# Performance work log

Measured on AMD Instinct MI355X. Metric: run time of the kernel, lower is better.

## Reference

```python
import jax, jax.numpy as jnp
import numpy as np

N_NODES = 100000
N_EDGES = 1600000
IN_DIM, HID_DIM, OUT_DIM = 128, 128, 64


def setup_inputs() -> dict:
    key = jax.random.key(0)
    ks = jax.random.split(key, 8)
    x = jax.random.normal(ks[0], (N_NODES, IN_DIM), dtype=jnp.float32)
    edge_index = jax.random.randint(ks[1], (2, N_EDGES), 0, N_NODES, dtype=jnp.int64)
    sc = 0.05
    W1 = jax.random.normal(ks[2], (IN_DIM, HID_DIM), dtype=jnp.float32) * sc
    b1 = jnp.zeros((HID_DIM,), dtype=jnp.float32)
    W2 = jax.random.normal(ks[3], (HID_DIM, HID_DIM), dtype=jnp.float32) * sc
    b2 = jnp.zeros((HID_DIM,), dtype=jnp.float32)
    W3 = jax.random.normal(ks[4], (HID_DIM, OUT_DIM), dtype=jnp.float32) * sc
    b3 = jnp.zeros((OUT_DIM,), dtype=jnp.float32)
    return {"x": x, "edge_index": edge_index, "W1": W1, "b1": b1,
            "W2": W2, "b2": b2, "W3": W3, "b3": b3}


def _gcn_conv(x, src, dst, norm, W, b, n_nodes):
    # x' = D^{-1/2} (A + I) D^{-1/2} (x W) + b   (PyG GCNConv default)
    h = x @ W                                   # [N, F_out]
    msg = h[src] * norm[:, None]                # gather + scale, [E+N, F_out]
    agg = jax.ops.segment_sum(msg, dst, num_segments=n_nodes)  # scatter-add
    return agg + b


def _build_norm(edge_index, n_nodes):
    # add self-loops, compute symmetric normalization coefficients
    loops = jnp.arange(n_nodes, dtype=edge_index.dtype)
    src = jnp.concatenate([edge_index[0], loops])
    dst = jnp.concatenate([edge_index[1], loops])
    deg = jax.ops.segment_sum(jnp.ones_like(dst, dtype=jnp.float32), dst,
                              num_segments=n_nodes)
    dinv = jnp.where(deg > 0, jax.lax.rsqrt(jnp.maximum(deg, 1.0)), 0.0)
    norm = dinv[src] * dinv[dst]
    return src, dst, norm


def reference(x, edge_index, W1, b1, W2, b2, W3, b3):
    n = x.shape[0]
    src, dst, norm = _build_norm(edge_index, n)
    h = jax.nn.relu(_gcn_conv(x, src, dst, norm, W1, b1, n))
    h = jax.nn.relu(_gcn_conv(h, src, dst, norm, W2, b2, n))
    out = _gcn_conv(h, src, dst, norm, W3, b3, n)
    return out
```

## Files before the change

### kernel.cpp

```cpp
#include <hip/hip_runtime.h>
#include <hip/hip_fp16.h>
#include <cstdint>
#include <cstddef>
#include <type_traits>

#define NN 100000
#define NE 1600000
#define SCAN_BLOCKS ((NN + 1023) / 1024)
#define NBK ((NN + 255) / 256)
#define BCAP 4608
#define EPB 4096
#define BIN_BLOCKS ((NE + EPB - 1) / EPB)

using half8 = __attribute__((ext_vector_type(8))) _Float16;
using f32x4 = __attribute__((ext_vector_type(4))) float;

union F4H8 { float4 f4; __half2 h2[4]; };

__device__ __forceinline__ uint2 pack4half(float4 v) {
    __half2 a = __floats2half2_rn(v.x, v.y);
    __half2 b = __floats2half2_rn(v.z, v.w);
    uint2 r;
    r.x = *(unsigned int*)&a;
    r.y = *(unsigned int*)&b;
    return r;
}

__global__ void detect_flag_kernel(const int* __restrict__ idx, int* __restrict__ flag) {
    __shared__ int cnt;
    if (threadIdx.x == 0) cnt = 0;
    __syncthreads();
    if (idx[2 * threadIdx.x + 1] == 0) atomicAdd(&cnt, 1);
    __syncthreads();
    if (threadIdx.x == 0) *flag = (cnt == (int)blockDim.x) ? 1 : 0;
}

__global__ __launch_bounds__(256) void bin_kernel(const void* __restrict__ idx,
                                                  const int* __restrict__ flag,
                                                  int* __restrict__ gcnt,
                                                  int* __restrict__ bucketbuf) {
    __shared__ int cnt[NBK];
    __shared__ int gbase[NBK];
    int t = threadIdx.x;
    long long base = (long long)blockIdx.x * EPB;
    for (int i = t; i < NBK; i += 256) cnt[i] = 0;
    __syncthreads();
    bool is64 = (*flag != 0);
    int lpos[16];
#pragma unroll
    for (int j = 0; j < 16; j++) {
        long long e = base + j * 256 + t;
        lpos[j] = 0;
        if (e < NE) {
            int d_ = is64 ? (int)((const long long*)idx)[NE + e]
                          : ((const int*)idx)[NE + e];
            lpos[j] = atomicAdd(&cnt[d_ >> 8], 1);
        }
    }
    __syncthreads();
    for (int b = t; b < NBK; b += 256) {
        int c = cnt[b];
        gbase[b] = (c > 0) ? atomicAdd(&gcnt[b * 16], c) : 0;
    }
    __syncthreads();
#pragma unroll
    for (int j = 0; j < 16; j++) {
        long long e = base + j * 256 + t;
        if (e < NE) {
            int s_, d_;
            if (is64) { const long long* p = (const long long*)idx; s_ = (int)p[e]; d_ = (int)p[NE + e]; }
            else      { const int* p = (const int*)idx;             s_ = p[e];      d_ = p[NE + e]; }
            int b = d_ >> 8;
            int pos = gbase[b] + lpos[j];
            if (pos < BCAP) bucketbuf[(size_t)b * BCAP + pos] = (s_ << 8) | (d_ & 255);
        }
    }
}

__global__ __launch_bounds__(256) void hist_kernel(const int* __restrict__ gcnt,
                                                   const int* __restrict__ bucketbuf,
                                                   int* __restrict__ deg) {
    __shared__ int cnt[256];
    int t = threadIdx.x, b = blockIdx.x;
    cnt[t] = 0;
    __syncthreads();
    int n = gcnt[b * 16]; if (n > BCAP) n = BCAP;
    for (int i = t; i < n; i += 256)
        atomicAdd(&cnt[bucketbuf[(size_t)b * BCAP + i] & 255], 1);
    __syncthreads();
    int node = b * 256 + t;
    if (node < NN) deg[node] = cnt[t];
}

__global__ void dinv_kernel(const int* __restrict__ deg, float* __restrict__ dinv) {
    int n = blockIdx.x * blockDim.x + threadIdx.x;
    if (n < NN) dinv[n] = rsqrtf((float)(deg[n] + 1));
}

__global__ __launch_bounds__(256) void scanA_kernel(const int* __restrict__ deg,
                                                    int* __restrict__ blocksum) {
    __shared__ int red[256];
    int t = threadIdx.x;
    int base = blockIdx.x * 1024 + t * 4;
    int s = 0;
#pragma unroll
    for (int j = 0; j < 4; j++) { int i = base + j; if (i < NN) s += deg[i]; }
    red[t] = s;
    __syncthreads();
    for (int off = 128; off > 0; off >>= 1) {
        if (t < off) red[t] += red[t + off];
        __syncthreads();
    }
    if (t == 0) blocksum[blockIdx.x] = red[0];
}

__global__ __launch_bounds__(256) void scanC_kernel(const int* __restrict__ deg,
                                                    const int* __restrict__ blocksum,
                                                    int* __restrict__ row_start) {
    __shared__ int lds[256];
    __shared__ int boff_s;
    int t = threadIdx.x;
    int b = blockIdx.x;
    lds[t] = (t < b && t < SCAN_BLOCKS) ? blocksum[t] : 0;
    __syncthreads();
    for (int off = 128; off > 0; off >>= 1) {
        if (t < off) lds[t] += lds[t + off];
        __syncthreads();
    }
    if (t == 0) boff_s = lds[0];
    __syncthreads();
    int boff = boff_s;

    int base = b * 1024 + t * 4;
    int d[4]; int s = 0;
#pragma unroll
    for (int j = 0; j < 4; j++) { int i = base + j; d[j] = (i < NN) ? deg[i] : 0; s += d[j]; }
    __syncthreads();
    lds[t] = s;
    __syncthreads();
    for (int off = 1; off < 256; off <<= 1) {
        int u = (t >= off) ? lds[t - off] : 0;
        __syncthreads();
        lds[t] += u;
        __syncthreads();
    }
    int offr = boff + ((t == 0) ? 0 : lds[t - 1]);
#pragma unroll
    for (int j = 0; j < 4; j++) {
        int i = base + j;
        if (i < NN) { row_start[i] = offr; offr += d[j]; }
    }
    if (b == 0 && t == 0) row_start[NN] = NE;
}

__global__ __launch_bounds__(256) void csrfill_kernel(const int* __restrict__ gcnt,
                                                      const int* __restrict__ bucketbuf,
                                                      const int* __restrict__ row_start,
                                                      int* __restrict__ csr) {
    __shared__ int cur[256];
    int t = threadIdx.x, b = blockIdx.x;
    int node = b * 256 + t;
    cur[t] = (node < NN) ? row_start[node] : 0;
    __syncthreads();
    int n = gcnt[b * 16]; if (n > BCAP) n = BCAP;
    for (int i = t; i < n; i += 256) {
        int v = bucketbuf[(size_t)b * BCAP + i];
        int pos = atomicAdd(&cur[v & 255], 1);
        csr[pos] = v >> 8;
    }
}

__global__ void wt_kernel(const float* __restrict__ W, __half* __restrict__ Wt, int F) {
    int i = blockIdx.x * 256 + threadIdx.x;
    if (i >= 128 * F) return;
    int k = i / F, n = i % F;
    Wt[(size_t)n * 128 + k] = __float2half(W[i]);
}

__global__ void xh_kernel(const float* __restrict__ X, __half* __restrict__ Xh) {
    int i = blockIdx.x * 256 + threadIdx.x;
    if (i >= NN * 128 / 4) return;
    float4 v = ((const float4*)X)[i];
    *(uint2*)&Xh[(size_t)i * 4] = pack4half(v);
}

template <int F>
__global__ __launch_bounds__(256) void mfma_gemm_kernel(const __half* __restrict__ A,
                                                        const __half* __restrict__ Wt,
                                                        const float* __restrict__ dinv,
                                                        __half* __restrict__ H, int N) {
    constexpr int K = 128;
    constexpr int NT = F / 16;
    constexpr int FP = F + 8;
    __shared__ __half hs[64 * FP];

    int wave = threadIdx.x >> 6;
    int lane = threadIdx.x & 63;
    int quad = lane >> 4;
    int l16  = lane & 15;
    int rowbase = blockIdx.x * 64 + wave * 16;
    int arow = rowbase + l16; if (arow >= N) arow = N - 1;

    half8 afrag[4];
    const __half* ap = A + (size_t)arow * K + quad * 8;
#pragma unroll
    for (int s = 0; s < 4; s++) afrag[s] = *(const half8*)(ap + s * 32);

    f32x4 acc[NT];
#pragma unroll
    for (int t = 0; t < NT; t++) acc[t] = (f32x4){0.f, 0.f, 0.f, 0.f};

#pragma unroll
    for (int s = 0; s < 4; s++) {
#pragma unroll
        for (int t = 0; t < NT; t++) {
            half8 b = *(const half8*)(Wt + (size_t)(t * 16 + l16) * K + s * 32 + quad * 8);
            acc[t] = __builtin_amdgcn_mfma_f32_16x16x32_f16(afrag[s], b, acc[t], 0, 0, 0);
        }
    }

    float dv[4];
#pragma unroll
    for (int r = 0; r < 4; r++) {
        int grow = rowbase + quad * 4 + r;
        dv[r] = (grow < N) ? dinv[grow] : 0.f;
    }
#pragma unroll
    for (int t = 0; t < NT; t++) {
#pragma unroll
        for (int r = 0; r < 4; r++) {
            int lrow = wave * 16 + quad * 4 + r;
            hs[lrow * FP + t * 16 + l16] = __float2half(acc[t][r] * dv[r]);
        }
    }
    __syncthreads();
    constexpr int CHUNKS = 64 * F / 8;
    for (int i = threadIdx.x; i < CHUNKS; i += 256) {
        int row = i / (F / 8);
        int col8 = (i % (F / 8)) * 8;
        int grow = blockIdx.x * 64 + row;
        if (grow < N)
            *(uint4*)&H[(size_t)grow * F + col8] = *(const uint4*)&hs[row * FP + col8];
    }
}

template <int F, bool RELU, typename OutT>
__global__ __launch_bounds__(256) void agg_kernel(const __half* __restrict__ Hs,
                                                  const int* __restrict__ rs,
                                                  const int* __restrict__ csr,
                                                  const float* __restrict__ dinv,
                                                  const float* __restrict__ bias,
                                                  OutT* __restrict__ OUT) {
    constexpr int CQ = F / 8;
    constexpr int NPB = 256 / CQ;
    int node = blockIdx.x * NPB + threadIdx.x / CQ;
    int q = (threadIdx.x % CQ) * 8;
    if (node >= NN) return;
    float dn = dinv[node];
    float acc[8];
    {
        F4H8 u; u.f4 = *(const float4*)&Hs[(size_t)node * F + q];
#pragma unroll
        for (int j = 0; j < 4; j++) {
            float2 f = __half22float2(u.h2[j]);
            acc[2 * j] = f.x; acc[2 * j + 1] = f.y;
        }
    }
    int e = rs[node];
    int e1 = rs[node + 1];
    for (; e + 8 <= e1; e += 8) {
        int s[8];
#pragma unroll
        for (int j = 0; j < 8; j++) s[j] = csr[e + j];
        F4H8 h[8];
#pragma unroll
        for (int j = 0; j < 8; j++) h[j].f4 = *(const float4*)&Hs[(size_t)s[j] * F + q];
#pragma unroll
        for (int j = 0; j < 8; j++) {
#pragma unroll
            for (int k = 0; k < 4; k++) {
                float2 f = __half22float2(h[j].h2[k]);
                acc[2 * k] += f.x; acc[2 * k + 1] += f.y;
            }
        }
    }
    for (; e < e1; e++) {
        int s = csr[e];
        F4H8 u; u.f4 = *(const float4*)&Hs[(size_t)s * F + q];
#pragma unroll
        for (int k = 0; k < 4; k++) {
            float2 f = __half22float2(u.h2[k]);
            acc[2 * k] += f.x; acc[2 * k + 1] += f.y;
        }
    }
    float o[8];
#pragma unroll
    for (int j = 0; j < 8; j++) {
        o[j] = dn * acc[j] + bias[q + j];
        if (RELU) o[j] = fmaxf(o[j], 0.f);
    }
    if constexpr (std::is_same<OutT, float>::value) {
        *(float4*)&OUT[(size_t)node * F + q]     = make_float4(o[0], o[1], o[2], o[3]);
        *(float4*)&OUT[(size_t)node * F + q + 4] = make_float4(o[4], o[5], o[6], o[7]);
    } else {
        uint4 p;
        uint2 a = pack4half(make_float4(o[0], o[1], o[2], o[3]));
        uint2 b = pack4half(make_float4(o[4], o[5], o[6], o[7]));
        p.x = a.x; p.y = a.y; p.z = b.x; p.w = b.y;
        *(uint4*)&OUT[(size_t)node * F + q] = p;
    }
}

extern "C" void kernel_launch(void* const* d_in, const int* in_sizes, int n_in,
                              void* d_out, int out_size, void* d_ws, size_t ws_size,
                              hipStream_t stream) {
    const float* x  = (const float*)d_in[0];
    const void* eidx = d_in[1];
    const float* W1 = (const float*)d_in[2];
    const float* b1 = (const float*)d_in[3];
    const float* W2 = (const float*)d_in[4];
    const float* b2 = (const float*)d_in[5];
    const float* W3 = (const float*)d_in[6];
    const float* b3 = (const float*)d_in[7];
    float* out = (float*)d_out;

    char* ws = (char*)d_ws;
    size_t off = 0;
    auto alloc = [&](size_t bytes) -> void* {
        void* p = ws + off;
        off += (bytes + 255) & ~(size_t)255;
        return p;
    };
    __half* bufB = (__half*)alloc((size_t)NN * 128 * 2);
    int* deg      = (int*)bufB;
    int* blocksum = (int*)((char*)bufB + (size_t)NN * 4);
    int* row_start = (int*)alloc((size_t)(NN + 1) * 4);
    float* dinv = (float*)alloc((size_t)NN * 4);
    int* flagp  = (int*)alloc(256);
    int* csr    = (int*)alloc((size_t)NE * 4);
    __half* bufH = (__half*)alloc((size_t)NN * 128 * 2);
    int* bucketbuf = (int*)bufH;
    int* gcnt      = (int*)((char*)bufH + (size_t)NBK * BCAP * 4);
    __half* Xh  = (__half*)alloc((size_t)NN * 128 * 2);
    __half* Wt1 = (__half*)alloc((size_t)128 * 128 * 2);
    __half* Wt2 = (__half*)alloc((size_t)128 * 128 * 2);
    __half* Wt3 = (__half*)alloc((size_t)64 * 128 * 2);

    hipMemsetAsync(gcnt, 0, (size_t)NBK * 16 * 4, stream);
    detect_flag_kernel<<<1, 256, 0, stream>>>((const int*)eidx, flagp);
    bin_kernel<<<BIN_BLOCKS, 256, 0, stream>>>(eidx, flagp, gcnt, bucketbuf);
    hist_kernel<<<NBK, 256, 0, stream>>>(gcnt, bucketbuf, deg);
    dinv_kernel<<<(NN + 255) / 256, 256, 0, stream>>>(deg, dinv);
    scanA_kernel<<<SCAN_BLOCKS, 256, 0, stream>>>(deg, blocksum);
    scanC_kernel<<<SCAN_BLOCKS, 256, 0, stream>>>(deg, blocksum, row_start);
    csrfill_kernel<<<NBK, 256, 0, stream>>>(gcnt, bucketbuf, row_start, csr);

    wt_kernel<<<(128 * 128 + 255) / 256, 256, 0, stream>>>(W1, Wt1, 128);
    wt_kernel<<<(128 * 128 + 255) / 256, 256, 0, stream>>>(W2, Wt2, 128);
    wt_kernel<<<(128 * 64 + 255) / 256, 256, 0, stream>>>(W3, Wt3, 64);
    xh_kernel<<<(NN * 128 / 4 + 255) / 256, 256, 0, stream>>>(x, Xh);

    const int GB = (NN + 63) / 64;
    mfma_gemm_kernel<128><<<GB, 256, 0, stream>>>(Xh, Wt1, dinv, bufH, NN);
    agg_kernel<128, true, __half><<<NN / 16, 256, 0, stream>>>(bufH, row_start, csr, dinv, b1, bufB);
    mfma_gemm_kernel<128><<<GB, 256, 0, stream>>>(bufB, Wt2, dinv, bufH, NN);
    agg_kernel<128, true, __half><<<NN / 16, 256, 0, stream>>>(bufH, row_start, csr, dinv, b2, bufB);
    mfma_gemm_kernel<64><<<GB, 256, 0, stream>>>(bufB, Wt3, dinv, bufH, NN);
    agg_kernel<64, false, float><<<NN / 32, 256, 0, stream>>>(bufH, row_start, csr, dinv, b3, out);
}
```

Measured before the change: 426.9 us.

## Sort nodes by degree for aggregation, fuse fp32 input conversion into GEMM

Builds a degree-bucketed node permutation (counting sort over 64 degree bins) during preprocessing. All three aggregation kernels then process nodes in that order, which reduces divergence among threads of a wave that handle nodes with different edge counts. The separate x-to-fp16 conversion pass is removed and the first GEMM reads fp32 directly and converts in registers. The dinv computation is also folded into the histogram kernel, and bin_kernel keeps dst indices in registers instead of reloading them. The cost is two extra small kernels plus an indirect order lookup, and output writes that are no longer coalesced across neighbouring nodes.

After: 424.8 us. No clear change (-0.5%).

```diff
diff --git a/kernel.cpp b/kernel.cpp
--- a/kernel.cpp
+++ b/kernel.cpp
@@ -11,6 +11,7 @@
 #define BCAP 4608
 #define EPB 4096
 #define BIN_BLOCKS ((NE + EPB - 1) / EPB)
+#define SBINS 64
 
 using half8 = __attribute__((ext_vector_type(8))) _Float16;
 using f32x4 = __attribute__((ext_vector_type(4))) float;
@@ -46,14 +47,15 @@
     for (int i = t; i < NBK; i += 256) cnt[i] = 0;
     __syncthreads();
     bool is64 = (*flag != 0);
-    int lpos[16];
+    int lpos[16], d16[16];
 #pragma unroll
     for (int j = 0; j < 16; j++) {
         long long e = base + j * 256 + t;
-        lpos[j] = 0;
+        lpos[j] = 0; d16[j] = 0;
         if (e < NE) {
             int d_ = is64 ? (int)((const long long*)idx)[NE + e]
                           : ((const int*)idx)[NE + e];
+            d16[j] = d_;
             lpos[j] = atomicAdd(&cnt[d_ >> 8], 1);
         }
     }
@@ -67,9 +69,8 @@
     for (int j = 0; j < 16; j++) {
         long long e = base + j * 256 + t;
         if (e < NE) {
-            int s_, d_;
-            if (is64) { const long long* p = (const long long*)idx; s_ = (int)p[e]; d_ = (int)p[NE + e]; }
-            else      { const int* p = (const int*)idx;             s_ = p[e];      d_ = p[NE + e]; }
+            int s_ = is64 ? (int)((const long long*)idx)[e] : ((const int*)idx)[e];
+            int d_ = d16[j];
             int b = d_ >> 8;
             int pos = gbase[b] + lpos[j];
             if (pos < BCAP) bucketbuf[(size_t)b * BCAP + pos] = (s_ << 8) | (d_ & 255);
@@ -79,22 +80,28 @@
 
 __global__ __launch_bounds__(256) void hist_kernel(const int* __restrict__ gcnt,
                                                    const int* __restrict__ bucketbuf,
-                                                   int* __restrict__ deg) {
+                                                   int* __restrict__ deg,
+                                                   float* __restrict__ dinv,
+                                                   int* __restrict__ scnt) {
     __shared__ int cnt[256];
+    __shared__ int sh[SBINS];
     int t = threadIdx.x, b = blockIdx.x;
     cnt[t] = 0;
+    if (t < SBINS) sh[t] = 0;
     __syncthreads();
     int n = gcnt[b * 16]; if (n > BCAP) n = BCAP;
     for (int i = t; i < n; i += 256)
         atomicAdd(&cnt[bucketbuf[(size_t)b * BCAP + i] & 255], 1);
     __syncthreads();
     int node = b * 256 + t;
-    if (node < NN) deg[node] = cnt[t];
-}
-
-__global__ void dinv_kernel(const int* __restrict__ deg, float* __restrict__ dinv) {
-    int n = blockIdx.x * blockDim.x + threadIdx.x;
-    if (n < NN) dinv[n] = rsqrtf((float)(deg[n] + 1));
+    if (node < NN) {
+        int d = cnt[t];
+        deg[node] = d;
+        dinv[node] = rsqrtf((float)(d + 1));
+        atomicAdd(&sh[d < SBINS ? d : SBINS - 1], 1);
+    }
+    __syncthreads();
+    if (t < SBINS && sh[t] > 0) atomicAdd(&scnt[t * 16], sh[t]);
 }
 
 __global__ __launch_bounds__(256) void scanA_kernel(const int* __restrict__ deg,
@@ -170,6 +177,38 @@
     }
 }
 
+__global__ void sort_scan_kernel(const int* __restrict__ scnt, int* __restrict__ sbase) {
+    if (threadIdx.x == 0) {
+        int acc = 0;
+        for (int i = 0; i < SBINS; i++) { sbase[i * 16] = acc; acc += scnt[i * 16]; }
+    }
+}
+
+__global__ __launch_bounds__(256) void order_kernel(const int* __restrict__ deg,
+                                                    int* __restrict__ sbase,
+                                                    int* __restrict__ order) {
+    __shared__ int lcnt[SBINS];
+    __shared__ int lbase[SBINS];
+    int t = threadIdx.x;
+    if (t < SBINS) lcnt[t] = 0;
+    __syncthreads();
+    int node = blockIdx.x * 256 + t;
+    int bin = 0, lpos = 0;
+    bool valid = node < NN;
+    if (valid) {
+        int d = deg[node];
+        bin = d < SBINS ? d : SBINS - 1;
+        lpos = atomicAdd(&lcnt[bin], 1);
+    }
+    __syncthreads();
+    if (t < SBINS) {
+        int c = lcnt[t];
+        lbase[t] = (c > 0) ? atomicAdd(&sbase[t * 16], c) : 0;
+    }
+    __syncthreads();
+    if (valid) order[lbase[bin] + lpos] = node;
+}
+
 __global__ void wt_kernel(const float* __restrict__ W, __half* __restrict__ Wt, int F) {
     int i = blockIdx.x * 256 + threadIdx.x;
     if (i >= 128 * F) return;
@@ -177,15 +216,8 @@
     Wt[(size_t)n * 128 + k] = __float2half(W[i]);
 }
 
-__global__ void xh_kernel(const float* __restrict__ X, __half* __restrict__ Xh) {
-    int i = blockIdx.x * 256 + threadIdx.x;
-    if (i >= NN * 128 / 4) return;
-    float4 v = ((const float4*)X)[i];
-    *(uint2*)&Xh[(size_t)i * 4] = pack4half(v);
-}
-
-template <int F>
-__global__ __launch_bounds__(256) void mfma_gemm_kernel(const __half* __restrict__ A,
+template <int F, typename AT>
+__global__ __launch_bounds__(256) void mfma_gemm_kernel(const AT* __restrict__ A,
                                                         const __half* __restrict__ Wt,
                                                         const float* __restrict__ dinv,
                                                         __half* __restrict__ H, int N) {
@@ -202,9 +234,22 @@
     int arow = rowbase + l16; if (arow >= N) arow = N - 1;
 
     half8 afrag[4];
-    const __half* ap = A + (size_t)arow * K + quad * 8;
-#pragma unroll
-    for (int s = 0; s < 4; s++) afrag[s] = *(const half8*)(ap + s * 32);
+    const AT* ap = A + (size_t)arow * K + quad * 8;
+#pragma unroll
+    for (int s = 0; s < 4; s++) {
+        if constexpr (std::is_same<AT, float>::value) {
+            float4 u0 = *(const float4*)(ap + s * 32);
+            float4 u1 = *(const float4*)(ap + s * 32 + 4);
+            half8 h;
+            h[0] = (_Float16)u0.x; h[1] = (_Float16)u0.y;
+            h[2] = (_Float16)u0.z; h[3] = (_Float16)u0.w;
+            h[4] = (_Float16)u1.x; h[5] = (_Float16)u1.y;
+            h[6] = (_Float16)u1.z; h[7] = (_Float16)u1.w;
+            afrag[s] = h;
+        } else {
+            afrag[s] = *(const half8*)(ap + s * 32);
+        }
+    }
 
     f32x4 acc[NT];
 #pragma unroll
@@ -246,6 +291,7 @@
 
 template <int F, bool RELU, typename OutT>
 __global__ __launch_bounds__(256) void agg_kernel(const __half* __restrict__ Hs,
+                                                  const int* __restrict__ order,
                                                   const int* __restrict__ rs,
                                                   const int* __restrict__ csr,
                                                   const float* __restrict__ dinv,
@@ -253,9 +299,10 @@
                                                   OutT* __restrict__ OUT) {
     constexpr int CQ = F / 8;
     constexpr int NPB = 256 / CQ;
-    int node = blockIdx.x * NPB + threadIdx.x / CQ;
+    int idx = blockIdx.x * NPB + threadIdx.x / CQ;
     int q = (threadIdx.x % CQ) * 8;
-    if (node >= NN) return;
+    if (idx >= NN) return;
+    int node = order[idx];
     float dn = dinv[node];
     float acc[8];
     {
@@ -341,30 +388,33 @@
     __half* bufH = (__half*)alloc((size_t)NN * 128 * 2);
     int* bucketbuf = (int*)bufH;
     int* gcnt      = (int*)((char*)bufH + (size_t)NBK * BCAP * 4);
-    __half* Xh  = (__half*)alloc((size_t)NN * 128 * 2);
     __half* Wt1 = (__half*)alloc((size_t)128 * 128 * 2);
     __half* Wt2 = (__half*)alloc((size_t)128 * 128 * 2);
     __half* Wt3 = (__half*)alloc((size_t)64 * 128 * 2);
+    int* scnt  = (int*)alloc(SBINS * 16 * 4);
+    int* sbase = (int*)alloc(SBINS * 16 * 4);
+    int* order = (int*)alloc((size_t)NN * 4);
 
     hipMemsetAsync(gcnt, 0, (size_t)NBK * 16 * 4, stream);
+    hipMemsetAsync(scnt, 0, SBINS * 16 * 4, stream);
     detect_flag_kernel<<<1, 256, 0, stream>>>((const int*)eidx, flagp);
     bin_kernel<<<BIN_BLOCKS, 256, 0, stream>>>(eidx, flagp, gcnt, bucketbuf);
-    hist_kernel<<<NBK, 256, 0, stream>>>(gcnt, bucketbuf, deg);
-    dinv_kernel<<<(NN + 255) / 256, 256, 0, stream>>>(deg, dinv);
+    hist_kernel<<<NBK, 256, 0, stream>>>(gcnt, bucketbuf, deg, dinv, scnt);
     scanA_kernel<<<SCAN_BLOCKS, 256, 0, stream>>>(deg, blocksum);
     scanC_kernel<<<SCAN_BLOCKS, 256, 0, stream>>>(deg, blocksum, row_start);
     csrfill_kernel<<<NBK, 256, 0, stream>>>(gcnt, bucketbuf, row_start, csr);
+    sort_scan_kernel<<<1, 64, 0, stream>>>(scnt, sbase);
+    order_kernel<<<NBK, 256, 0, stream>>>(deg, sbase, order);
 
     wt_kernel<<<(128 * 128 + 255) / 256, 256, 0, stream>>>(W1, Wt1, 128);
     wt_kernel<<<(128 * 128 + 255) / 256, 256, 0, stream>>>(W2, Wt2, 128);
     wt_kernel<<<(128 * 64 + 255) / 256, 256, 0, stream>>>(W3, Wt3, 64);
-    xh_kernel<<<(NN * 128 / 4 + 255) / 256, 256, 0, stream>>>(x, Xh);
 
     const int GB = (NN + 63) / 64;
-    mfma_gemm_kernel<128><<<GB, 256, 0, stream>>>(Xh, Wt1, dinv, bufH, NN);
-    agg_kernel<128, true, __half><<<NN / 16, 256, 0, stream>>>(bufH, row_start, csr, dinv, b1, bufB);
-    mfma_gemm_kernel<128><<<GB, 256, 0, stream>>>(bufB, Wt2, dinv, bufH, NN);
-    agg_kernel<128, true, __half><<<NN / 16, 256, 0, stream>>>(bufH, row_start, csr, dinv, b2, bufB);
-    mfma_gemm_kernel<64><<<GB, 256, 0, stream>>>(bufB, Wt3, dinv, bufH, NN);
-    agg_kernel<64, false, float><<<NN / 32, 256, 0, stream>>>(bufH, row_start, csr, dinv, b3, out);
-}
+    mfma_gemm_kernel<128, float><<<GB, 256, 0, stream>>>(x, Wt1, dinv, bufH, NN);
+    agg_kernel<128, true, __half><<<NN / 16, 256, 0, stream>>>(bufH, order, row_start, csr, dinv, b1, bufB);
+    mfma_gemm_kernel<128, __half><<<GB, 256, 0, stream>>>(bufB, Wt2, dinv, bufH, NN);
+    agg_kernel<128, true, __half><<<NN / 16, 256, 0, stream>>>(bufH, order, row_start, csr, dinv, b2, bufB);
+    mfma_gemm_kernel<64, __half><<<GB, 256, 0, stream>>>(bufB, Wt3, dinv, bufH, NN);
+    agg_kernel<64, false, float><<<NN / 32, 256, 0, stream>>>(bufH, order, row_start, csr, dinv, b3, out);
+}
```

## Fuse aggregation with next-layer GEMM and fold fp16 conversion into first GEMM

Applied to the files above, without the earlier changes.

Hidden-layer aggregation is fused with the following layer's MFMA GEMM. Aggregated rows are staged in LDS, so the intermediate activation never makes a round trip through global memory. The x-to-fp16 conversion kernel is removed by converting fp32 rows inside the first GEMM's fragment load, and the dinv computation is folded into the histogram kernel. The bin kernel now keeps src/dst in registers instead of reloading them. The cost is a fused kernel that runs 64 nodes per block with 16 threads per node doing the gather, which may lower occupancy and memory-level parallelism compared with the standalone aggregation kernel.

New measurement: 398.8 us. 6.6% less time.

```diff
diff --git a/kernel.cpp b/kernel.cpp
--- a/kernel.cpp
+++ b/kernel.cpp
@@ -46,40 +46,40 @@
     for (int i = t; i < NBK; i += 256) cnt[i] = 0;
     __syncthreads();
     bool is64 = (*flag != 0);
-    int lpos[16];
+    int lpos[16], d16[16], s16[16];
 #pragma unroll
     for (int j = 0; j < 16; j++) {
         long long e = base + j * 256 + t;
-        lpos[j] = 0;
-        if (e < NE) {
-            int d_ = is64 ? (int)((const long long*)idx)[NE + e]
-                          : ((const int*)idx)[NE + e];
-            lpos[j] = atomicAdd(&cnt[d_ >> 8], 1);
-        }
-    }
-    __syncthreads();
-    for (int b = t; b < NBK; b += 256) {
-        int c = cnt[b];
-        gbase[b] = (c > 0) ? atomicAdd(&gcnt[b * 16], c) : 0;
-    }
-    __syncthreads();
-#pragma unroll
-    for (int j = 0; j < 16; j++) {
-        long long e = base + j * 256 + t;
+        lpos[j] = 0; d16[j] = 0; s16[j] = 0;
         if (e < NE) {
             int s_, d_;
             if (is64) { const long long* p = (const long long*)idx; s_ = (int)p[e]; d_ = (int)p[NE + e]; }
             else      { const int* p = (const int*)idx;             s_ = p[e];      d_ = p[NE + e]; }
-            int b = d_ >> 8;
+            d16[j] = d_; s16[j] = s_;
+            lpos[j] = atomicAdd(&cnt[d_ >> 8], 1);
+        }
+    }
+    __syncthreads();
+    for (int b = t; b < NBK; b += 256) {
+        int c = cnt[b];
+        gbase[b] = (c > 0) ? atomicAdd(&gcnt[b * 16], c) : 0;
+    }
+    __syncthreads();
+#pragma unroll
+    for (int j = 0; j < 16; j++) {
+        long long e = base + j * 256 + t;
+        if (e < NE) {
+            int b = d16[j] >> 8;
             int pos = gbase[b] + lpos[j];
-            if (pos < BCAP) bucketbuf[(size_t)b * BCAP + pos] = (s_ << 8) | (d_ & 255);
+            if (pos < BCAP) bucketbuf[(size_t)b * BCAP + pos] = (s16[j] << 8) | (d16[j] & 255);
         }
     }
 }
 
 __global__ __launch_bounds__(256) void hist_kernel(const int* __restrict__ gcnt,
                                                    const int* __restrict__ bucketbuf,
-                                                   int* __restrict__ deg) {
+                                                   int* __restrict__ deg,
+                                                   float* __restrict__ dinv) {
     __shared__ int cnt[256];
     int t = threadIdx.x, b = blockIdx.x;
     cnt[t] = 0;
@@ -89,12 +89,11 @@
         atomicAdd(&cnt[bucketbuf[(size_t)b * BCAP + i] & 255], 1);
     __syncthreads();
     int node = b * 256 + t;
-    if (node < NN) deg[node] = cnt[t];
-}
-
-__global__ void dinv_kernel(const int* __restrict__ deg, float* __restrict__ dinv) {
-    int n = blockIdx.x * blockDim.x + threadIdx.x;
-    if (n < NN) dinv[n] = rsqrtf((float)(deg[n] + 1));
+    if (node < NN) {
+        int d = cnt[t];
+        deg[node] = d;
+        dinv[node] = rsqrtf((float)(d + 1));
+    }
 }
 
 __global__ __launch_bounds__(256) void scanA_kernel(const int* __restrict__ deg,
@@ -177,15 +176,8 @@
     Wt[(size_t)n * 128 + k] = __float2half(W[i]);
 }
 
-__global__ void xh_kernel(const float* __restrict__ X, __half* __restrict__ Xh) {
-    int i = blockIdx.x * 256 + threadIdx.x;
-    if (i >= NN * 128 / 4) return;
-    float4 v = ((const float4*)X)[i];
-    *(uint2*)&Xh[(size_t)i * 4] = pack4half(v);
-}
-
-template <int F>
-__global__ __launch_bounds__(256) void mfma_gemm_kernel(const __half* __restrict__ A,
+template <int F, typename AT>
+__global__ __launch_bounds__(256) void mfma_gemm_kernel(const AT* __restrict__ A,
                                                         const __half* __restrict__ Wt,
                                                         const float* __restrict__ dinv,
                                                         __half* __restrict__ H, int N) {
@@ -202,9 +194,22 @@
     int arow = rowbase + l16; if (arow >= N) arow = N - 1;
 
     half8 afrag[4];
-    const __half* ap = A + (size_t)arow * K + quad * 8;
-#pragma unroll
-    for (int s = 0; s < 4; s++) afrag[s] = *(const half8*)(ap + s * 32);
+    const AT* ap = A + (size_t)arow * K + quad * 8;
+#pragma unroll
+    for (int s = 0; s < 4; s++) {
+        if constexpr (std::is_same<AT, float>::value) {
+            float4 u0 = *(const float4*)(ap + s * 32);
+            float4 u1 = *(const float4*)(ap + s * 32 + 4);
+            half8 h;
+            h[0] = (_Float16)u0.x; h[1] = (_Float16)u0.y;
+            h[2] = (_Float16)u0.z; h[3] = (_Float16)u0.w;
+            h[4] = (_Float16)u1.x; h[5] = (_Float16)u1.y;
+            h[6] = (_Float16)u1.z; h[7] = (_Float16)u1.w;
+            afrag[s] = h;
+        } else {
+            afrag[s] = *(const half8*)(ap + s * 32);
+        }
+    }
 
     f32x4 acc[NT];
 #pragma unroll
@@ -244,13 +249,135 @@
     }
 }
 
-template <int F, bool RELU, typename OutT>
+template <int FO>
+__global__ __launch_bounds__(256) void agg_gemm_kernel(const __half* __restrict__ Hs,
+                                                       const int* __restrict__ rs,
+                                                       const int* __restrict__ csr,
+                                                       const float* __restrict__ dinv,
+                                                       const float* __restrict__ bias,
+                                                       const __half* __restrict__ Wt,
+                                                       __half* __restrict__ Hout) {
+    constexpr int FI = 128;
+    constexpr int FP = FI + 8;
+    constexpr int NT = FO / 16;
+    __shared__ __half Alds[64 * FP];
+
+    int tid = threadIdx.x;
+    int nodebase = blockIdx.x * 64;
+
+#pragma unroll
+    for (int pass = 0; pass < 4; pass++) {
+        int lrow = pass * 16 + tid / 16;
+        int node = nodebase + lrow;
+        int q = (tid % 16) * 8;
+        float acc[8];
+        if (node < NN) {
+            float dn = dinv[node];
+            {
+                F4H8 u; u.f4 = *(const float4*)&Hs[(size_t)node * FI + q];
+#pragma unroll
+                for (int j = 0; j < 4; j++) {
+                    float2 f = __half22float2(u.h2[j]);
+                    acc[2 * j] = f.x; acc[2 * j + 1] = f.y;
+                }
+            }
+            int e = rs[node];
+            int e1 = rs[node + 1];
+            for (; e + 8 <= e1; e += 8) {
+                int s[8];
+#pragma unroll
+                for (int j = 0; j < 8; j++) s[j] = csr[e + j];
+                F4H8 h[8];
+#pragma unroll
+                for (int j = 0; j < 8; j++) h[j].f4 = *(const float4*)&Hs[(size_t)s[j] * FI + q];
+#pragma unroll
+                for (int j = 0; j < 8; j++) {
+#pragma unroll
+                    for (int k = 0; k < 4; k++) {
+                        float2 f = __half22float2(h[j].h2[k]);
+                        acc[2 * k] += f.x; acc[2 * k + 1] += f.y;
+                    }
+                }
+            }
+            for (; e < e1; e++) {
+                int s = csr[e];
+                F4H8 u; u.f4 = *(const float4*)&Hs[(size_t)s * FI + q];
+#pragma unroll
+                for (int k = 0; k < 4; k++) {
+                    float2 f = __half22float2(u.h2[k]);
+                    acc[2 * k] += f.x; acc[2 * k + 1] += f.y;
+                }
+            }
+#pragma unroll
+            for (int j = 0; j < 8; j++)
+                acc[j] = fmaxf(dn * acc[j] + bias[q + j], 0.f);
+        } else {
+#pragma unroll
+            for (int j = 0; j < 8; j++) acc[j] = 0.f;
+        }
+        uint4 p;
+        uint2 a = pack4half(make_float4(acc[0], acc[1], acc[2], acc[3]));
+        uint2 b = pack4half(make_float4(acc[4], acc[5], acc[6], acc[7]));
+        p.x = a.x; p.y = a.y; p.z = b.x; p.w = b.y;
+        *(uint4*)&Alds[lrow * FP + q] = p;
+    }
+    __syncthreads();
+
+    int wave = tid >> 6;
+    int lane = tid & 63;
+    int quad = lane >> 4;
+    int l16  = lane & 15;
+    int rowbase = nodebase + wave * 16;
+
+    half8 afrag[4];
+#pragma unroll
+    for (int s = 0; s < 4; s++)
+        afrag[s] = *(const half8*)&Alds[(wave * 16 + l16) * FP + s * 32 + quad * 8];
+
+    f32x4 acc[NT];
+#pragma unroll
+    for (int t = 0; t < NT; t++) acc[t] = (f32x4){0.f, 0.f, 0.f, 0.f};
+#pragma unroll
+    for (int s = 0; s < 4; s++) {
+#pragma unroll
+        for (int t = 0; t < NT; t++) {
+            half8 b = *(const half8*)(Wt + (size_t)(t * 16 + l16) * FI + s * 32 + quad * 8);
+            acc[t] = __builtin_amdgcn_mfma_f32_16x16x32_f16(afrag[s], b, acc[t], 0, 0, 0);
+        }
+    }
+
+    float dv[4];
+#pragma unroll
+    for (int r = 0; r < 4; r++) {
+        int grow = rowbase + quad * 4 + r;
+        dv[r] = (grow < NN) ? dinv[grow] : 0.f;
+    }
+#pragma unroll
+    for (int t = 0; t < NT; t++) {
+#pragma unroll
+        for (int r = 0; r < 4; r++) {
+            int lrow = wave * 16 + quad * 4 + r;
+            Alds[lrow * FP + t * 16 + l16] = __float2half(acc[t][r] * dv[r]);
+        }
+    }
+    __syncthreads();
+    constexpr int CHUNKS = 64 * FO / 8;
+    for (int i = tid; i < CHUNKS; i += 256) {
+        int row = i / (FO / 8);
+        int col8 = (i % (FO / 8)) * 8;
+        int grow = nodebase + row;
+        if (grow < NN)
+            *(uint4*)&Hout[(size_t)grow * FO + col8] = *(const uint4*)&Alds[row * FP + col8];
+    }
+}
+
+template <int F>
 __global__ __launch_bounds__(256) void agg_kernel(const __half* __restrict__ Hs,
                                                   const int* __restrict__ rs,
                                                   const int* __restrict__ csr,
                                                   const float* __restrict__ dinv,
                                                   const float* __restrict__ bias,
-                                                  OutT* __restrict__ OUT) {
+                                                  float* __restrict__ OUT) {
     constexpr int CQ = F / 8;
     constexpr int NPB = 256 / CQ;
     int node = blockIdx.x * NPB + threadIdx.x / CQ;
@@ -293,22 +420,12 @@
             acc[2 * k] += f.x; acc[2 * k + 1] += f.y;
         }
     }
-    float o[8];
-#pragma unroll
-    for (int j = 0; j < 8; j++) {
-        o[j] = dn * acc[j] + bias[q + j];
-        if (RELU) o[j] = fmaxf(o[j], 0.f);
-    }
-    if constexpr (std::is_same<OutT, float>::value) {
-        *(float4*)&OUT[(size_t)node * F + q]     = make_float4(o[0], o[1], o[2], o[3]);
-        *(float4*)&OUT[(size_t)node * F + q + 4] = make_float4(o[4], o[5], o[6], o[7]);
-    } else {
-        uint4 p;
-        uint2 a = pack4half(make_float4(o[0], o[1], o[2], o[3]));
-        uint2 b = pack4half(make_float4(o[4], o[5], o[6], o[7]));
-        p.x = a.x; p.y = a.y; p.z = b.x; p.w = b.y;
-        *(uint4*)&OUT[(size_t)node * F + q] = p;
-    }
+    float4 o0 = make_float4(dn * acc[0] + bias[q],     dn * acc[1] + bias[q + 1],
+                            dn * acc[2] + bias[q + 2], dn * acc[3] + bias[q + 3]);
+    float4 o1 = make_float4(dn * acc[4] + bias[q + 4], dn * acc[5] + bias[q + 5],
+                            dn * acc[6] + bias[q + 6], dn * acc[7] + bias[q + 7]);
+    *(float4*)&OUT[(size_t)node * F + q]     = o0;
+    *(float4*)&OUT[(size_t)node * F + q + 4] = o1;
 }
 
 extern "C" void kernel_launch(void* const* d_in, const int* in_sizes, int n_in,
@@ -331,17 +448,16 @@
         off += (bytes + 255) & ~(size_t)255;
         return p;
     };
-    __half* bufB = (__half*)alloc((size_t)NN * 128 * 2);
-    int* deg      = (int*)bufB;
-    int* blocksum = (int*)((char*)bufB + (size_t)NN * 4);
+    __half* bufA = (__half*)alloc((size_t)NN * 128 * 2);
+    int* bucketbuf = (int*)bufA;
+    int* gcnt      = (int*)((char*)bufA + (size_t)NBK * BCAP * 4);
+    __half* bufC = (__half*)alloc((size_t)NN * 128 * 2);
+    int* deg      = (int*)bufC;
+    int* blocksum = (int*)((char*)bufC + (size_t)NN * 4);
     int* row_start = (int*)alloc((size_t)(NN + 1) * 4);
     float* dinv = (float*)alloc((size_t)NN * 4);
     int* flagp  = (int*)alloc(256);
     int* csr    = (int*)alloc((size_t)NE * 4);
-    __half* bufH = (__half*)alloc((size_t)NN * 128 * 2);
-    int* bucketbuf = (int*)bufH;
-    int* gcnt      = (int*)((char*)bufH + (size_t)NBK * BCAP * 4);
-    __half* Xh  = (__half*)alloc((size_t)NN * 128 * 2);
     __half* Wt1 = (__half*)alloc((size_t)128 * 128 * 2);
     __half* Wt2 = (__half*)alloc((size_t)128 * 128 * 2);
     __half* Wt3 = (__half*)alloc((size_t)64 * 128 * 2);
@@ -349,8 +465,7 @@
     hipMemsetAsync(gcnt, 0, (size_t)NBK * 16 * 4, stream);
     detect_flag_kernel<<<1, 256, 0, stream>>>((const int*)eidx, flagp);
     bin_kernel<<<BIN_BLOCKS, 256, 0, stream>>>(eidx, flagp, gcnt, bucketbuf);
-    hist_kernel<<<NBK, 256, 0, stream>>>(gcnt, bucketbuf, deg);
-    dinv_kernel<<<(NN + 255) / 256, 256, 0, stream>>>(deg, dinv);
+    hist_kernel<<<NBK, 256, 0, stream>>>(gcnt, bucketbuf, deg, dinv);
     scanA_kernel<<<SCAN_BLOCKS, 256, 0, stream>>>(deg, blocksum);
     scanC_kernel<<<SCAN_BLOCKS, 256, 0, stream>>>(deg, blocksum, row_start);
     csrfill_kernel<<<NBK, 256, 0, stream>>>(gcnt, bucketbuf, row_start, csr);
@@ -358,13 +473,10 @@
     wt_kernel<<<(128 * 128 + 255) / 256, 256, 0, stream>>>(W1, Wt1, 128);
     wt_kernel<<<(128 * 128 + 255) / 256, 256, 0, stream>>>(W2, Wt2, 128);
     wt_kernel<<<(128 * 64 + 255) / 256, 256, 0, stream>>>(W3, Wt3, 64);
-    xh_kernel<<<(NN * 128 / 4 + 255) / 256, 256, 0, stream>>>(x, Xh);
 
     const int GB = (NN + 63) / 64;
-    mfma_gemm_kernel<128><<<GB, 256, 0, stream>>>(Xh, Wt1, dinv, bufH, NN);
-    agg_kernel<128, true, __half><<<NN / 16, 256, 0, stream>>>(bufH, row_start, csr, dinv, b1, bufB);
-    mfma_gemm_kernel<128><<<GB, 256, 0, stream>>>(bufB, Wt2, dinv, bufH, NN);
-    agg_kernel<128, true, __half><<<NN / 16, 256, 0, stream>>>(bufH, row_start, csr, dinv, b2, bufB);
-    mfma_gemm_kernel<64><<<GB, 256, 0, stream>>>(bufB, Wt3, dinv, bufH, NN);
-    agg_kernel<64, false, float><<<NN / 32, 256, 0, stream>>>(bufH, row_start, csr, dinv, b3, out);
-}
+    mfma_gemm_kernel<128, float><<<GB, 256, 0, stream>>>(x, Wt1, dinv, bufA, NN);
+    agg_gemm_kernel<128><<<GB, 256, 0, stream>>>(bufA, row_start, csr, dinv, b1, Wt2, bufC);
+    agg_gemm_kernel<64><<<GB, 256, 0, stream>>>(bufC, row_start, csr, dinv, b2, Wt3, bufA);
+    agg_kernel<64><<<NN / 32, 256, 0, stream>>>(bufA, row_start, csr, dinv, b3, out);
+}
```
